# Performance work log

Measured on AMD Instinct MI355X. Metric: run time of the kernel, lower is better.

Reference implementation:

```python
import jax, jax.numpy as jnp
import numpy as np

B, T, C, H, N = 4, 1024, 2048, 32, 64
DFF, DW, DV, DA, DG = 8192, 64, 32, 64, 128
GN_EPS = 64e-5  # RWKV7 ln_x GroupNorm eps


def _ln(x, w, b, eps=1e-5):
    m = x.mean(-1, keepdims=True)
    v = ((x - m) ** 2).mean(-1, keepdims=True)
    return (x - m) / jnp.sqrt(v + eps) * w + b


def _block(x, v_first, att_shift, ffn_shift, wkv_state,
           ln1_w, ln1_b, ln2_w, ln2_b,
           x_r, x_w, x_k, x_v, x_a, x_g,
           Wr, Wk, Wv, Wo,
           w0, w1, w2, v0, v1, v2, a0, a1, a2, g1, g2,
           k_k, k_a, r_k, lnx_w, lnx_b,
           ffn_xk, Wk_ffn, Wv_ffn):
    # ----- TimeMix -----
    xn = _ln(x, ln1_w, ln1_b)
    xx = jnp.concatenate([att_shift[:, None, :], xn[:, :-1]], axis=1) - xn
    xr = xn + xx * x_r
    xw = xn + xx * x_w
    xk_ = xn + xx * x_k
    xv = xn + xx * x_v
    xa = xn + xx * x_a
    xg = xn + xx * x_g

    r = xr @ Wr
    w = -jax.nn.softplus(-(w0 + jnp.tanh(xw @ w1) @ w2)) - 0.5  # <= -0.5
    k = xk_ @ Wk
    v = xv @ Wv
    # layer_id != 0: interpolate toward v_first
    v = v + (v_first - v) * jax.nn.sigmoid(v0 + (xv @ v1) @ v2)
    a = jax.nn.sigmoid(a0 + (xa @ a1) @ a2)
    g = jax.nn.sigmoid(xg @ g1) @ g2

    kk = (k * k_k).reshape(B, T, H, N)
    kk = kk / jnp.maximum(jnp.linalg.norm(kk, axis=-1, keepdims=True), 1e-12)
    k = k * (1.0 + (a - 1.0) * k_a)

    rh = r.reshape(B, T, H, N)
    wh = jnp.exp(-jnp.exp(w.reshape(B, T, H, N)))  # decay in (0,1)
    kh = k.reshape(B, T, H, N)
    vh = v.reshape(B, T, H, N)
    ah = a.reshape(B, T, H, N)
    aa = -kk
    bb = kk * ah

    def step(S, inp):
        # S: [B,H,N(value),N(key)]
        r_t, w_t, k_t, v_t, a_t, b_t = inp
        sa = jnp.einsum('bhvk,bhk->bhv', S, a_t)
        S = S * w_t[:, :, None, :] + sa[..., None] * b_t[:, :, None, :] + v_t[..., None] * k_t[:, :, None, :]
        y = jnp.einsum('bhvk,bhk->bhv', S, r_t)
        return S, y

    tm = lambda z: jnp.swapaxes(z, 0, 1)  # [B,T,H,N] -> [T,B,H,N]
    S_new, ys = jax.lax.scan(step, wkv_state, (tm(rh), tm(wh), tm(kh), tm(vh), tm(aa), tm(bb)))
    x_wkv = jnp.swapaxes(ys, 0, 1).reshape(B, T, C)

    # GroupNorm over H groups of size N (RWKV7 ln_x)
    xh = x_wkv.reshape(B, T, H, N)
    mu = xh.mean(-1, keepdims=True)
    var = ((xh - mu) ** 2).mean(-1, keepdims=True)
    x_wkv = ((xh - mu) / jnp.sqrt(var + GN_EPS)).reshape(B, T, C) * lnx_w + lnx_b

    resid = ((rh * kh * r_k).sum(-1, keepdims=True) * vh).reshape(B, T, C)
    x_wkv = x_wkv + resid
    att_out = (x_wkv * g) @ Wo
    x1 = x + att_out

    # ----- ChannelMix -----
    xn2 = _ln(x1, ln2_w, ln2_b)
    xx2 = jnp.concatenate([ffn_shift[:, None, :], xn2[:, :-1]], axis=1) - xn2
    xkf = xn2 + xx2 * ffn_xk
    kf = jnp.square(jax.nn.relu(xkf @ Wk_ffn))
    x_out = x1 + kf @ Wv_ffn
    return x_out, S_new


def setup_inputs() -> dict:
    ks = jax.random.split(jax.random.key(0), 48)
    rn = lambda i, sh, s=1.0: jax.random.normal(ks[i], sh, dtype=jnp.float32) * s
    return {
        'x': rn(0, (B, T, C)), 'v_first': rn(1, (B, T, C)),
        'att_shift': rn(2, (B, C)), 'ffn_shift': rn(3, (B, C)),
        'wkv_state': jnp.zeros((B, H, N, N), jnp.float32),
        'ln1_w': jnp.ones((C,), jnp.float32), 'ln1_b': jnp.zeros((C,), jnp.float32),
        'ln2_w': jnp.ones((C,), jnp.float32), 'ln2_b': jnp.zeros((C,), jnp.float32),
        'x_r': rn(4, (C,), 0.3), 'x_w': rn(5, (C,), 0.3), 'x_k': rn(6, (C,), 0.3),
        'x_v': rn(7, (C,), 0.3), 'x_a': rn(8, (C,), 0.3), 'x_g': rn(9, (C,), 0.3),
        'Wr': rn(10, (C, C), 0.02), 'Wk': rn(11, (C, C), 0.02),
        'Wv': rn(12, (C, C), 0.02), 'Wo': rn(13, (C, C), 0.02),
        'w0': rn(14, (C,), 0.3), 'w1': rn(15, (C, DW), 0.02), 'w2': rn(16, (DW, C), 0.02),
        'v0': rn(17, (C,), 0.3), 'v1': rn(18, (C, DV), 0.02), 'v2': rn(19, (DV, C), 0.02),
        'a0': rn(20, (C,), 0.3), 'a1': rn(21, (C, DA), 0.02), 'a2': rn(22, (DA, C), 0.02),
        'g1': rn(23, (C, DG), 0.02), 'g2': rn(24, (DG, C), 0.02),
        'k_k': rn(25, (C,), 0.1) + 0.7, 'k_a': rn(26, (C,), 0.1) + 0.7, 'r_k': rn(27, (H, N), 0.1),
        'lnx_w': jnp.ones((C,), jnp.float32), 'lnx_b': jnp.zeros((C,), jnp.float32),
        'ffn_xk': rn(28, (C,), 0.3), 'Wk_ffn': rn(29, (C, DFF), 0.02), 'Wv_ffn': rn(30, (DFF, C), 0.02),
    }


def reference(x, v_first, att_shift, ffn_shift, wkv_state,
              ln1_w, ln1_b, ln2_w, ln2_b,
              x_r, x_w, x_k, x_v, x_a, x_g,
              Wr, Wk, Wv, Wo,
              w0, w1, w2, v0, v1, v2, a0, a1, a2, g1, g2,
              k_k, k_a, r_k, lnx_w, lnx_b,
              ffn_xk, Wk_ffn, Wv_ffn):
    return _block(x, v_first, att_shift, ffn_shift, wkv_state,
                  ln1_w, ln1_b, ln2_w, ln2_b,
                  x_r, x_w, x_k, x_v, x_a, x_g,
                  Wr, Wk, Wv, Wo,
                  w0, w1, w2, v0, v1, v2, a0, a1, a2, g1, g2,
                  k_k, k_a, r_k, lnx_w, lnx_b,
                  ffn_xk, Wk_ffn, Wv_ffn)
```

## Files before the change

kernel.cpp:

```cpp
#include <hip/hip_runtime.h>
#include <cstdint>


typedef __attribute__((ext_vector_type(4))) float f32x4;
typedef __attribute__((ext_vector_type(8))) __bf16 bf16x8;
typedef __attribute__((ext_vector_type(8))) unsigned short us8;

#define DEV __device__ __forceinline__

DEV unsigned short f2b(float f) {
  union { float f; unsigned u; } v; v.f = f;
  unsigned r = v.u + 0x7fffu + ((v.u >> 16) & 1u);
  return (unsigned short)(r >> 16);
}
DEV float b2f(unsigned short u) {
  union { unsigned u; float f; } v; v.u = (unsigned)u << 16;
  return v.f;
}

DEV void gload16(const void* g, void* l) {
  void* gg = const_cast<void*>(g);
  __builtin_amdgcn_global_load_lds(
      (__attribute__((address_space(1))) unsigned int*)gg,
      (__attribute__((address_space(3))) unsigned int*)l, 16, 0, 0);
}

DEV float red8(float v) {
  v += __shfl_xor(v, 1);
  v += __shfl_xor(v, 2);
  v += __shfl_xor(v, 4);
  return v;
}


__global__ void k_transpose(const float* __restrict__ src,
                            unsigned short* __restrict__ dst, int R, int Cc) {
  __shared__ float tile[32][33];
  const int c0 = blockIdx.x * 32, r0 = blockIdx.y * 32;
  const int tx = threadIdx.x, ty = threadIdx.y;
  for (int i = ty; i < 32; i += 8)
    tile[i][tx] = src[(size_t)(r0 + i) * Cc + c0 + tx];
  __syncthreads();
  for (int i = ty; i < 32; i += 8)
    dst[(size_t)(c0 + i) * R + r0 + tx] = f2b(tile[tx][i]);
}

__global__ void k_wcat(const float* __restrict__ w1, const float* __restrict__ a1,
                       const float* __restrict__ v1, const float* __restrict__ g1,
                       const float* __restrict__ xw, const float* __restrict__ xa,
                       const float* __restrict__ xv, const float* __restrict__ xg,
                       unsigned short* __restrict__ dst) {
  const int i = blockIdx.x * 256 + threadIdx.x;
  if (i >= 384 * 4096) return;
  const int j = i >> 12, c = i & 4095;
  float val = 0.f;
  if (j < 288) {
    const float* W; const float* mix; int jj, D;
    if (j < 64)       { W = w1; mix = xw; jj = j;       D = 64;  }
    else if (j < 128) { W = a1; mix = xa; jj = j - 64;  D = 64;  }
    else if (j < 160) { W = v1; mix = xv; jj = j - 128; D = 32;  }
    else              { W = g1; mix = xg; jj = j - 160; D = 128; }
    const int cc = c & 2047;
    val = W[(size_t)cc * D + jj];
    if (c >= 2048) val *= mix[cc];
  }
  dst[i] = f2b(val);
}


DEV void breduce2(float& a, float& b, float* rbuf) {
#pragma unroll
  for (int m = 1; m < 64; m <<= 1) { a += __shfl_xor(a, m); b += __shfl_xor(b, m); }
  const int wid = threadIdx.x >> 6, lane = threadIdx.x & 63;
  if (lane == 0) { rbuf[wid] = a; rbuf[4 + wid] = b; }
  __syncthreads();
  a = rbuf[0] + rbuf[1] + rbuf[2] + rbuf[3];
  b = rbuf[4] + rbuf[5] + rbuf[6] + rbuf[7];
  __syncthreads();
}

__global__ __launch_bounds__(256)
void k_ln1_mix(const float* __restrict__ x, const float* __restrict__ shift,
               const float* __restrict__ lw, const float* __restrict__ lb,
               const float* __restrict__ mr, const float* __restrict__ mk,
               const float* __restrict__ mv,
               unsigned short* __restrict__ A2, unsigned short* __restrict__ xrb,
               unsigned short* __restrict__ xkb, unsigned short* __restrict__ xvb) {
  __shared__ float rbuf[8];
  const int m = blockIdx.x, tid = threadIdx.x;
  const int b = m >> 10, t = m & 1023;
  const float* xt = x + (size_t)m * 2048 + tid * 8;
  const float* xp = (t > 0) ? (x + (size_t)(m - 1) * 2048 + tid * 8)
                            : (shift + (size_t)b * 2048 + tid * 8);
  float vt[8], vp[8];
  *(float4*)&vt[0] = *(const float4*)(xt);
  *(float4*)&vt[4] = *(const float4*)(xt + 4);
  *(float4*)&vp[0] = *(const float4*)(xp);
  *(float4*)&vp[4] = *(const float4*)(xp + 4);
  float st = 0.f, sp = 0.f;
#pragma unroll
  for (int i = 0; i < 8; ++i) { st += vt[i]; sp += vp[i]; }
  breduce2(st, sp, rbuf);
  const float mt_ = st * (1.f / 2048.f), mp_ = sp * (1.f / 2048.f);
  float qt = 0.f, qp = 0.f;
#pragma unroll
  for (int i = 0; i < 8; ++i) {
    float d0 = vt[i] - mt_; qt += d0 * d0;
    float d1 = vp[i] - mp_; qp += d1 * d1;
  }
  breduce2(qt, qp, rbuf);
  const float rt = rsqrtf(qt * (1.f / 2048.f) + 1e-5f);
  const float rp = rsqrtf(qp * (1.f / 2048.f) + 1e-5f);
  const bool lnp = (t > 0);
#pragma unroll
  for (int i = 0; i < 8; ++i) {
    const int c = tid * 8 + i;
    const float wv = lw[c], bv = lb[c];
    const float xn = (vt[i] - mt_) * rt * wv + bv;
    const float pn = lnp ? ((vp[i] - mp_) * rp * wv + bv) : vp[i];
    const float xx = pn - xn;
    A2[(size_t)m * 4096 + c] = f2b(xn);
    A2[(size_t)m * 4096 + 2048 + c] = f2b(xx);
    xrb[(size_t)m * 2048 + c] = f2b(xn + xx * mr[c]);
    xkb[(size_t)m * 2048 + c] = f2b(xn + xx * mk[c]);
    xvb[(size_t)m * 2048 + c] = f2b(xn + xx * mv[c]);
  }
}

__global__ __launch_bounds__(256)
void k_ln2_mix(const float* __restrict__ x1, const float* __restrict__ shift,
               const float* __restrict__ lw, const float* __restrict__ lb,
               const float* __restrict__ mk, unsigned short* __restrict__ xkf) {
  __shared__ float rbuf[8];
  const int m = blockIdx.x, tid = threadIdx.x;
  const int b = m >> 10, t = m & 1023;
  const float* xt = x1 + (size_t)m * 2048 + tid * 8;
  const float* xp = (t > 0) ? (x1 + (size_t)(m - 1) * 2048 + tid * 8)
                            : (shift + (size_t)b * 2048 + tid * 8);
  float vt[8], vp[8];
  *(float4*)&vt[0] = *(const float4*)(xt);
  *(float4*)&vt[4] = *(const float4*)(xt + 4);
  *(float4*)&vp[0] = *(const float4*)(xp);
  *(float4*)&vp[4] = *(const float4*)(xp + 4);
  float st = 0.f, sp = 0.f;
#pragma unroll
  for (int i = 0; i < 8; ++i) { st += vt[i]; sp += vp[i]; }
  breduce2(st, sp, rbuf);
  const float mt_ = st * (1.f / 2048.f), mp_ = sp * (1.f / 2048.f);
  float qt = 0.f, qp = 0.f;
#pragma unroll
  for (int i = 0; i < 8; ++i) {
    float d0 = vt[i] - mt_; qt += d0 * d0;
    float d1 = vp[i] - mp_; qp += d1 * d1;
  }
  breduce2(qt, qp, rbuf);
  const float rt = rsqrtf(qt * (1.f / 2048.f) + 1e-5f);
  const float rp = rsqrtf(qp * (1.f / 2048.f) + 1e-5f);
  const bool lnp = (t > 0);
#pragma unroll
  for (int i = 0; i < 8; ++i) {
    const int c = tid * 8 + i;
    const float wv = lw[c], bv = lb[c];
    const float xn = (vt[i] - mt_) * rt * wv + bv;
    const float pn = lnp ? ((vp[i] - mp_) * rp * wv + bv) : vp[i];
    xkf[(size_t)m * 2048 + c] = f2b(xn + (pn - xn) * mk[c]);
  }
}


constexpr int EP_F32 = 0, EP_B16 = 1, EP_W = 2, EP_AB16 = 3, EP_VGB16 = 4,
              EP_RELU2 = 5, EP_ADDF = 6, EP_HACT = 7;

template <int EP>
DEV void ep_store(float acc, long row, long c, long ldc, float* Co,
                  unsigned short* Cob, const float* bias, const float* e0f,
                  const unsigned short* e0b) {
  const long idx = row * ldc + c;
  if constexpr (EP == EP_F32) {
    Co[idx] = acc;
  } else if constexpr (EP == EP_B16) {
    Cob[idx] = f2b(acc);
  } else if constexpr (EP == EP_W) {
    const float wv = bias[c] + acc;
    const float sp = log1pf(expf(-wv));
    const float w = -sp - 0.5f;
    Co[idx] = expf(-expf(w));
  } else if constexpr (EP == EP_AB16) {
    Cob[idx] = f2b(1.f / (1.f + expf(-(bias[c] + acc))));
  } else if constexpr (EP == EP_VGB16) {
    const float s = 1.f / (1.f + expf(-(bias[c] + acc)));
    const float vv = b2f(e0b[idx]);
    Cob[idx] = f2b(vv + (e0f[idx] - vv) * s);
  } else if constexpr (EP == EP_RELU2) {
    const float r = fmaxf(acc, 0.f);
    Cob[idx] = f2b(r * r);
  } else if constexpr (EP == EP_ADDF) {
    Co[idx] = acc + e0f[idx];
  } else if constexpr (EP == EP_HACT) {
    float vv = acc;
    if (c < 64) vv = tanhf(vv);
    else if (c >= 160) vv = 1.f / (1.f + expf(-vv));
    Cob[idx] = f2b(vv);
  }
}

template <int EP>
__global__ __launch_bounds__(256)
void gemm_bt(const unsigned short* __restrict__ A, long lda,
             const unsigned short* __restrict__ Bt, long ldb, long N, long K,
             long ldc, float* __restrict__ Co, unsigned short* __restrict__ Cob,
             const float* __restrict__ bias, const float* __restrict__ e0f,
             const unsigned short* __restrict__ e0b) {
  __shared__ unsigned short As[4096];
  __shared__ unsigned short Bs[4096];
  const int tid = threadIdx.x;
  const int wid = tid >> 6, lane = tid & 63;
  const long row0 = (long)blockIdx.x * 128, col0 = (long)blockIdx.y * 128;
  const int wm = (wid >> 1) * 64, wn = (wid & 1) * 64;
  f32x4 acc[4][4] = {};
  const int sr = tid >> 2, sk = (tid & 3) * 8;
  const unsigned short* gA = A + (row0 + sr) * lda + sk;
  const unsigned short* gB = Bt + (col0 + sr) * ldb + sk;
  unsigned short* lA = As + wid * 512;
  unsigned short* lB = Bs + wid * 512;
  const int fr = lane & 15, fk = (lane >> 4) * 8;

  for (long kb = 0; kb < K; kb += 32) {
    gload16(gA + kb, lA);
    gload16(gA + kb + 64 * lda, lA + 2048);
    gload16(gB + kb, lB);
    gload16(gB + kb + 64 * ldb, lB + 2048);
    __syncthreads();
    bf16x8 af[4], bq[4];
#pragma unroll
    for (int mt = 0; mt < 4; ++mt)
      af[mt] = *(const bf16x8*)(As + (wm + mt * 16 + fr) * 32 + fk);
#pragma unroll
    for (int nt = 0; nt < 4; ++nt)
      bq[nt] = *(const bf16x8*)(Bs + (wn + nt * 16 + fr) * 32 + fk);
#pragma unroll
    for (int mt = 0; mt < 4; ++mt)
#pragma unroll
      for (int nt = 0; nt < 4; ++nt)
        acc[mt][nt] = __builtin_amdgcn_mfma_f32_16x16x32_bf16(
            af[mt], bq[nt], acc[mt][nt], 0, 0, 0);
    __syncthreads();
  }
  const int fq = lane >> 4;
#pragma unroll
  for (int mt = 0; mt < 4; ++mt) {
#pragma unroll
    for (int nt = 0; nt < 4; ++nt) {
      const long c = col0 + wn + nt * 16 + fr;
      if (c < N) {
        const long rb = row0 + wm + mt * 16 + fq * 4;
#pragma unroll
        for (int rg = 0; rg < 4; ++rg)
          ep_store<EP>(acc[mt][nt][rg], rb + rg, c, ldc, Co, Cob, bias, e0f, e0b);
      }
    }
  }
}

__global__ __launch_bounds__(256)
void k_post(unsigned short* __restrict__ kio, unsigned short* __restrict__ abio,
            unsigned short* __restrict__ aao, const float* __restrict__ kkw,
            const float* __restrict__ kaw) {
  const int m = blockIdx.x, tid = threadIdx.x;
  const size_t base = (size_t)m * 2048 + tid * 8;
  us8 k8 = *(const us8*)(kio + base);
  us8 a8 = *(const us8*)(abio + base);
  float kk8[8], ka8[8];
  *(float4*)&kk8[0] = *(const float4*)(kkw + tid * 8);
  *(float4*)&kk8[4] = *(const float4*)(kkw + tid * 8 + 4);
  *(float4*)&ka8[0] = *(const float4*)(kaw + tid * 8);
  *(float4*)&ka8[4] = *(const float4*)(kaw + tid * 8 + 4);
  float kx[8], kv[8], av[8];
  float ss = 0.f;
#pragma unroll
  for (int i = 0; i < 8; ++i) {
    kv[i] = b2f(k8[i]); av[i] = b2f(a8[i]);
    kx[i] = kv[i] * kk8[i]; ss += kx[i] * kx[i];
  }
  ss = red8(ss);
  const float inv = 1.f / fmaxf(sqrtf(ss), 1e-12f);
  us8 kh8, aa8, bb8;
#pragma unroll
  for (int i = 0; i < 8; ++i) {
    const float kkn = kx[i] * inv;
    kh8[i] = f2b(kv[i] * (1.f + (av[i] - 1.f) * ka8[i]));
    aa8[i] = f2b(-kkn);
    bb8[i] = f2b(kkn * av[i]);
  }
  *(us8*)(kio + base) = kh8;
  *(us8*)(aao + base) = aa8;
  *(us8*)(abio + base) = bb8;
}


DEV float red16(float x) {
  union { float f; int i; } a, r;
  a.f = x; r.i = __builtin_amdgcn_update_dpp(0, a.i, 0xB1, 0xf, 0xf, true);
  x += r.f;
  a.f = x; r.i = __builtin_amdgcn_update_dpp(0, a.i, 0x4E, 0xf, 0xf, true);
  x += r.f;
  a.f = x; r.i = __builtin_amdgcn_update_dpp(0, a.i, 0x124, 0xf, 0xf, true);
  x += r.f;
  a.f = x; r.i = __builtin_amdgcn_update_dpp(0, a.i, 0x128, 0xf, 0xf, true);
  x += r.f;
  return x;
}

DEV void cv4(const uint2 q, float* o) {
  union { unsigned u; float f; } t;
  t.u = q.x << 16;          o[0] = t.f;
  t.u = q.x & 0xffff0000u;  o[1] = t.f;
  t.u = q.y << 16;          o[2] = t.f;
  t.u = q.y & 0xffff0000u;  o[3] = t.f;
}

__global__ __launch_bounds__(64)
void k_scan(const unsigned short* __restrict__ rp,
            const unsigned short* __restrict__ kp,
            const unsigned short* __restrict__ vp,
            const float* __restrict__ wp,
            const unsigned short* __restrict__ ap,
            const unsigned short* __restrict__ bp,
            const float* __restrict__ s0, float* __restrict__ yout,
            float* __restrict__ snew) {
  __shared__ float ylds[1024][4];
  const int lane = threadIdx.x;
  const int bh = blockIdx.x & 127;
  const int rq = blockIdx.x >> 7;
  const int b = bh >> 5, h = bh & 31;
  const int kg = lane & 15, rl = lane >> 4;
  const int v = rq * 4 + rl, ks = kg * 4;
  const size_t off_bh = (size_t)b * 1024 * 2048 + (size_t)h * 64;

  const unsigned short* prb = rp + off_bh + ks;
  const unsigned short* pkb = kp + off_bh + ks;
  const unsigned short* pab = ap + off_bh + ks;
  const unsigned short* pbb = bp + off_bh + ks;
  const float*          pwb = wp + off_bh + ks;
  const unsigned short* pvb = vp + off_bh + v;

  float S[4];
  *(float4*)&S[0] = *(const float4*)(s0 + (((size_t)bh * 64 + v) * 64 + ks));

  uint2 r0_, k0_, a0_, b0_, r1_, k1_, a1_, b1_;
  uint2 r2_, k2_, a2_, b2_, r3_, k3_, a3_, b3_;
  uint2 r4_, k4_, a4_, b4_, r5_, k5_, a5_, b5_;
  uint2 r6_, k6_, a6_, b6_, r7_, k7_, a7_, b7_;
  float4 w0_, w1_, w2_, w3_, w4_, w5_, w6_, w7_;
  unsigned short f0_, f1_, f2_, f3_, f4_, f5_, f6_, f7_;

#define SLOAD(Br, Bk, Ba, Bb, Bw, Bf, T)                                     \
  {                                                                          \
    const size_t o_ = (size_t)(T) * 2048;                                    \
    Br = *(const uint2*)(prb + o_);  Bk = *(const uint2*)(pkb + o_);         \
    Ba = *(const uint2*)(pab + o_);  Bb = *(const uint2*)(pbb + o_);         \
    Bw = *(const float4*)(pwb + o_); Bf = pvb[o_];                           \
  }

  SLOAD(r0_, k0_, a0_, b0_, w0_, f0_, 0)
  SLOAD(r1_, k1_, a1_, b1_, w1_, f1_, 1)
  SLOAD(r2_, k2_, a2_, b2_, w2_, f2_, 2)
  SLOAD(r3_, k3_, a3_, b3_, w3_, f3_, 3)
  SLOAD(r4_, k4_, a4_, b4_, w4_, f4_, 4)
  SLOAD(r5_, k5_, a5_, b5_, w5_, f5_, 5)
  SLOAD(r6_, k6_, a6_, b6_, w6_, f6_, 6)
  SLOAD(r7_, k7_, a7_, b7_, w7_, f7_, 7)

#define SBODY(T, Br, Bk, Ba, Bb, Bw, Bf)                                     \
  {                                                                          \
    float rr[4], kk[4], av[4], bv[4];                                        \
    cv4(Br, rr); cv4(Bk, kk); cv4(Ba, av); cv4(Bb, bv);                      \
    const float4 wf = Bw;                                                    \
    const float vv = b2f(Bf);                                                \
    int tn_ = (T) + 8; if (tn_ > 1023) tn_ = 1023;                           \
    SLOAD(Br, Bk, Ba, Bb, Bw, Bf, tn_)                                       \
    float sa = S[0] * av[0] + S[1] * av[1] + S[2] * av[2] + S[3] * av[3];    \
    sa = red16(sa);                                                          \
    float y;                                                                 \
    S[0] = S[0] * wf.x + sa * bv[0] + vv * kk[0]; y  = S[0] * rr[0];         \
    S[1] = S[1] * wf.y + sa * bv[1] + vv * kk[1]; y += S[1] * rr[1];         \
    S[2] = S[2] * wf.z + sa * bv[2] + vv * kk[2]; y += S[2] * rr[2];         \
    S[3] = S[3] * wf.w + sa * bv[3] + vv * kk[3]; y += S[3] * rr[3];         \
    y = red16(y);                                                            \
    if (kg == 0) ylds[T][rl] = y;                                            \
  }

  for (int tb = 0; tb < 1024; tb += 8) {
    SBODY(tb + 0, r0_, k0_, a0_, b0_, w0_, f0_)
    SBODY(tb + 1, r1_, k1_, a1_, b1_, w1_, f1_)
    SBODY(tb + 2, r2_, k2_, a2_, b2_, w2_, f2_)
    SBODY(tb + 3, r3_, k3_, a3_, b3_, w3_, f3_)
    SBODY(tb + 4, r4_, k4_, a4_, b4_, w4_, f4_)
    SBODY(tb + 5, r5_, k5_, a5_, b5_, w5_, f5_)
    SBODY(tb + 6, r6_, k6_, a6_, b6_, w6_, f6_)
    SBODY(tb + 7, r7_, k7_, a7_, b7_, w7_, f7_)
  }
#undef SBODY
#undef SLOAD

  *(float4*)(snew + (((size_t)bh * 64 + v) * 64 + ks)) = *(const float4*)&S[0];
  __syncthreads();
#pragma unroll 4
  for (int it = 0; it < 16; ++it) {
    const int t = lane + it * 64;
    *(float4*)(yout + off_bh + (size_t)t * 2048 + rq * 4) =
        *(const float4*)&ylds[t][0];
  }
}


__global__ __launch_bounds__(256)
void k_gn(const float* __restrict__ y, const unsigned short* __restrict__ r,
          const unsigned short* __restrict__ kh, const unsigned short* __restrict__ vf,
          const unsigned short* __restrict__ g, const float* __restrict__ rk,
          const float* __restrict__ lw, const float* __restrict__ lb,
          unsigned short* __restrict__ ywg) {
  const int m = blockIdx.x, tid = threadIdx.x;
  const size_t base = (size_t)m * 2048 + tid * 8;
  float yv[8];
  *(float4*)&yv[0] = *(const float4*)(y + base);
  *(float4*)&yv[4] = *(const float4*)(y + base + 4);
  us8 r8 = *(const us8*)(r + base);
  us8 k8 = *(const us8*)(kh + base);
  us8 v8 = *(const us8*)(vf + base);
  us8 g8 = *(const us8*)(g + base);
  float rkv[8];
  *(float4*)&rkv[0] = *(const float4*)(rk + tid * 8);
  *(float4*)&rkv[4] = *(const float4*)(rk + tid * 8 + 4);
  float sy = 0.f, sd = 0.f;
#pragma unroll
  for (int i = 0; i < 8; ++i) {
    sy += yv[i];
    sd += b2f(r8[i]) * b2f(k8[i]) * rkv[i];
  }
  sy = red8(sy);
  sd = red8(sd);
  const float mu = sy * (1.f / 64.f);
  float sq = 0.f;
#pragma unroll
  for (int i = 0; i < 8; ++i) { const float d = yv[i] - mu; sq += d * d; }
  sq = red8(sq);
  const float rstd = rsqrtf(sq * (1.f / 64.f) + 64e-5f);
  us8 o8;
#pragma unroll
  for (int i = 0; i < 8; ++i) {
    const int c = tid * 8 + i;
    const float gn = (yv[i] - mu) * rstd * lw[c] + lb[c];
    o8[i] = f2b((gn + sd * b2f(v8[i])) * b2f(g8[i]));
  }
  *(us8*)(ywg + base) = o8;
}


extern "C" void kernel_launch(void* const* d_in, const int* in_sizes, int n_in,
                              void* d_out, int out_size, void* d_ws,
                              size_t ws_size, hipStream_t stream) {
  (void)in_sizes; (void)n_in; (void)out_size; (void)ws_size;
  const float* x         = (const float*)d_in[0];
  const float* v_first   = (const float*)d_in[1];
  const float* att_shift = (const float*)d_in[2];
  const float* ffn_shift = (const float*)d_in[3];
  const float* wkv0      = (const float*)d_in[4];
  const float* ln1w = (const float*)d_in[5];
  const float* ln1b = (const float*)d_in[6];
  const float* ln2w = (const float*)d_in[7];
  const float* ln2b = (const float*)d_in[8];
  const float* x_r = (const float*)d_in[9];
  const float* x_w = (const float*)d_in[10];
  const float* x_k = (const float*)d_in[11];
  const float* x_v = (const float*)d_in[12];
  const float* x_a = (const float*)d_in[13];
  const float* x_g = (const float*)d_in[14];
  const float* Wr = (const float*)d_in[15];
  const float* Wk = (const float*)d_in[16];
  const float* Wv = (const float*)d_in[17];
  const float* Wo = (const float*)d_in[18];
  const float* w0 = (const float*)d_in[19];
  const float* w1 = (const float*)d_in[20];
  const float* w2 = (const float*)d_in[21];
  const float* v0 = (const float*)d_in[22];
  const float* v1 = (const float*)d_in[23];
  const float* v2 = (const float*)d_in[24];
  const float* a0 = (const float*)d_in[25];
  const float* a1 = (const float*)d_in[26];
  const float* a2 = (const float*)d_in[27];
  const float* g1 = (const float*)d_in[28];
  const float* g2 = (const float*)d_in[29];
  const float* k_k = (const float*)d_in[30];
  const float* k_a = (const float*)d_in[31];
  const float* r_k = (const float*)d_in[32];
  const float* lnxw = (const float*)d_in[33];
  const float* lnxb = (const float*)d_in[34];
  const float* ffn_xk = (const float*)d_in[35];
  const float* Wkf = (const float*)d_in[36];
  const float* Wvf = (const float*)d_in[37];

  char* ws = (char*)d_ws;
  constexpr size_t OFF_TWR   = 0;
  constexpr size_t OFF_TWK   = 8388608;
  constexpr size_t OFF_TWV   = 16777216;
  constexpr size_t OFF_TWO   = 25165824;
  constexpr size_t OFF_TW2   = 33554432;
  constexpr size_t OFF_TA2   = 33816576;
  constexpr size_t OFF_TV2   = 34078720;
  constexpr size_t OFF_TG2   = 34209792;
  constexpr size_t OFF_TWCAT = 34734080;
  constexpr size_t OFF_HACT  = 37879808;
  constexpr size_t OFF_GBUF  = 40239104;
  constexpr size_t OFF_WH    = 57016320;
  constexpr size_t OFF_R     = 90570752;
  constexpr size_t OFF_KH    = 107347968;
  constexpr size_t OFF_VF    = 124125184;
  constexpr size_t OFF_AA    = 140902400;
  constexpr size_t OFF_BB    = 157679616;

  unsigned short* tWr = (unsigned short*)(ws + OFF_TWR);
  unsigned short* tWk = (unsigned short*)(ws + OFF_TWK);
  unsigned short* tWv = (unsigned short*)(ws + OFF_TWV);
  unsigned short* tWo = (unsigned short*)(ws + OFF_TWO);
  unsigned short* tw2 = (unsigned short*)(ws + OFF_TW2);
  unsigned short* ta2 = (unsigned short*)(ws + OFF_TA2);
  unsigned short* tv2 = (unsigned short*)(ws + OFF_TV2);
  unsigned short* tg2 = (unsigned short*)(ws + OFF_TG2);
  unsigned short* tWcat = (unsigned short*)(ws + OFF_TWCAT);
  unsigned short* Hact  = (unsigned short*)(ws + OFF_HACT);
  unsigned short* gbuf  = (unsigned short*)(ws + OFF_GBUF);
  unsigned short* tWvfh = (unsigned short*)(ws + OFF_GBUF);
  unsigned short* act2  = (unsigned short*)(ws + OFF_WH);
  float*          whb   = (float*)(ws + OFF_WH);
  unsigned short* ywg   = (unsigned short*)(ws + OFF_WH);
  unsigned short* kf    = (unsigned short*)(ws + OFF_WH);
  unsigned short* bxr   = (unsigned short*)(ws + OFF_AA);
  unsigned short* bxk   = (unsigned short*)(ws + OFF_BB);
  unsigned short* bxv   = (unsigned short*)(ws + OFF_VF);
  unsigned short* rbuf  = (unsigned short*)(ws + OFF_R);
  unsigned short* khb   = (unsigned short*)(ws + OFF_KH);
  unsigned short* vfb   = (unsigned short*)(ws + OFF_VF);
  unsigned short* aab   = (unsigned short*)(ws + OFF_AA);
  unsigned short* bbb   = (unsigned short*)(ws + OFF_BB);
  unsigned short* vraw  = (unsigned short*)(ws + OFF_AA);
  unsigned short* abuf  = (unsigned short*)(ws + OFF_BB);
  float*          x1    = (float*)(ws + OFF_R);
  unsigned short* xkf   = (unsigned short*)(ws + OFF_VF);
  unsigned short* tWkf  = (unsigned short*)(ws + OFF_AA);
  float* out = (float*)d_out;
  float* snew = out + 8388608;

  const dim3 tb(32, 8);
  k_transpose<<<dim3(64, 64), tb, 0, stream>>>(Wr, tWr, 2048, 2048);
  k_transpose<<<dim3(64, 64), tb, 0, stream>>>(Wk, tWk, 2048, 2048);
  k_transpose<<<dim3(64, 64), tb, 0, stream>>>(Wv, tWv, 2048, 2048);
  k_transpose<<<dim3(64, 64), tb, 0, stream>>>(Wo, tWo, 2048, 2048);
  k_transpose<<<dim3(64, 2), tb, 0, stream>>>(w2, tw2, 64, 2048);
  k_transpose<<<dim3(64, 2), tb, 0, stream>>>(a2, ta2, 64, 2048);
  k_transpose<<<dim3(64, 1), tb, 0, stream>>>(v2, tv2, 32, 2048);
  k_transpose<<<dim3(64, 4), tb, 0, stream>>>(g2, tg2, 128, 2048);
  k_wcat<<<6144, 256, 0, stream>>>(w1, a1, v1, g1, x_w, x_a, x_v, x_g, tWcat);

  k_ln1_mix<<<4096, 256, 0, stream>>>(x, att_shift, ln1w, ln1b, x_r, x_k, x_v,
                                      act2, bxr, bxk, bxv);
  gemm_bt<EP_B16><<<dim3(32, 16), 256, 0, stream>>>(
      bxr, 2048, tWr, 2048, 2048, 2048, 2048, nullptr, rbuf, nullptr, nullptr, nullptr);
  gemm_bt<EP_B16><<<dim3(32, 16), 256, 0, stream>>>(
      bxk, 2048, tWk, 2048, 2048, 2048, 2048, nullptr, khb, nullptr, nullptr, nullptr);
  gemm_bt<EP_B16><<<dim3(32, 16), 256, 0, stream>>>(
      bxv, 2048, tWv, 2048, 2048, 2048, 2048, nullptr, vraw, nullptr, nullptr, nullptr);
  gemm_bt<EP_HACT><<<dim3(32, 3), 256, 0, stream>>>(
      act2, 4096, tWcat, 4096, 288, 4096, 288, nullptr, Hact, nullptr, nullptr, nullptr);
  gemm_bt<EP_W><<<dim3(32, 16), 256, 0, stream>>>(
      Hact + 0, 288, tw2, 64, 2048, 64, 2048, whb, nullptr, w0, nullptr, nullptr);
  gemm_bt<EP_AB16><<<dim3(32, 16), 256, 0, stream>>>(
      Hact + 64, 288, ta2, 64, 2048, 64, 2048, nullptr, abuf, a0, nullptr, nullptr);
  gemm_bt<EP_VGB16><<<dim3(32, 16), 256, 0, stream>>>(
      Hact + 128, 288, tv2, 32, 2048, 32, 2048, nullptr, vfb, v0, v_first, vraw);
  gemm_bt<EP_B16><<<dim3(32, 16), 256, 0, stream>>>(
      Hact + 160, 288, tg2, 128, 2048, 128, 2048, nullptr, gbuf, nullptr, nullptr, nullptr);
  k_post<<<4096, 256, 0, stream>>>(khb, abuf, aab, k_k, k_a);

  k_scan<<<2048, 64, 0, stream>>>(rbuf, khb, vfb, whb, aab, bbb, wkv0, out, snew);
  k_gn<<<4096, 256, 0, stream>>>(out, rbuf, khb, vfb, gbuf, r_k, lnxw, lnxb, ywg);

  gemm_bt<EP_ADDF><<<dim3(32, 16), 256, 0, stream>>>(
      ywg, 2048, tWo, 2048, 2048, 2048, 2048, x1, nullptr, nullptr, x, nullptr);

  k_ln2_mix<<<4096, 256, 0, stream>>>(x1, ffn_shift, ln2w, ln2b, ffn_xk, xkf);
  k_transpose<<<dim3(256, 64), tb, 0, stream>>>(Wkf, tWkf, 2048, 8192);
  gemm_bt<EP_RELU2><<<dim3(32, 32), 256, 0, stream>>>(
      xkf, 2048, tWkf, 2048, 4096, 2048, 4096, nullptr, kf, nullptr, nullptr, nullptr);
  k_transpose<<<dim3(64, 128), tb, 0, stream>>>(Wvf, tWvfh, 4096, 2048);
  gemm_bt<EP_ADDF><<<dim3(32, 16), 256, 0, stream>>>(
      kf, 4096, tWvfh, 4096, 2048, 4096, 2048, out, nullptr, nullptr, x1, nullptr);
  gemm_bt<EP_RELU2><<<dim3(32, 32), 256, 0, stream>>>(
      xkf, 2048, tWkf + (size_t)4096 * 2048, 2048, 4096, 2048, 4096, nullptr, kf,
      nullptr, nullptr, nullptr);
  k_transpose<<<dim3(64, 128), tb, 0, stream>>>(Wvf + (size_t)4096 * 2048, tWvfh,
                                                4096, 2048);
  gemm_bt<EP_ADDF><<<dim3(32, 16), 256, 0, stream>>>(
      kf, 4096, tWvfh, 4096, 2048, 4096, 2048, out, nullptr, nullptr, out, nullptr);
}
```

Baseline: 1.416 ms.

## Stage scan inputs through LDS with async global_load_lds ring and bf16 output

The WKV scan kernel now prefetches each timestep's r/k/a/b/w/v rows into an 8-deep LDS ring with 49 lanes issuing 16-byte global_load_lds requests. This replaces the per-lane register prefetch of 8 timesteps and cuts the scattered small per-lane global loads and register pressure. The scan output y is also stored as bf16 instead of fp32, which halves the traffic into the GroupNorm kernel. The cost is an LDS round trip per step with manual waitcnt synchronization, which relies on wave-level ordering and drops the __syncthreads, plus reduced precision on y before normalization.

```diff
diff --git a/kernel.cpp b/kernel.cpp
--- a/kernel.cpp
+++ b/kernel.cpp
@@ -326,9 +326,10 @@
             const float* __restrict__ wp,
             const unsigned short* __restrict__ ap,
             const unsigned short* __restrict__ bp,
-            const float* __restrict__ s0, float* __restrict__ yout,
+            const float* __restrict__ s0, unsigned short* __restrict__ yout,
             float* __restrict__ snew) {
-  __shared__ float ylds[1024][4];
+  __shared__ float4 slots[8][49];
+  __shared__ unsigned short ylds[1024][4];
   const int lane = threadIdx.x;
   const int bh = blockIdx.x & 127;
   const int rq = blockIdx.x >> 7;
@@ -337,104 +338,93 @@
   const int v = rq * 4 + rl, ks = kg * 4;
   const size_t off_bh = (size_t)b * 1024 * 2048 + (size_t)h * 64;
 
-  const unsigned short* prb = rp + off_bh + ks;
-  const unsigned short* pkb = kp + off_bh + ks;
-  const unsigned short* pab = ap + off_bh + ks;
-  const unsigned short* pbb = bp + off_bh + ks;
-  const float*          pwb = wp + off_bh + ks;
-  const unsigned short* pvb = vp + off_bh + v;
-
   float S[4];
   *(float4*)&S[0] = *(const float4*)(s0 + (((size_t)bh * 64 + v) * 64 + ks));
 
-  uint2 r0_, k0_, a0_, b0_, r1_, k1_, a1_, b1_;
-  uint2 r2_, k2_, a2_, b2_, r3_, k3_, a3_, b3_;
-  uint2 r4_, k4_, a4_, b4_, r5_, k5_, a5_, b5_;
-  uint2 r6_, k6_, a6_, b6_, r7_, k7_, a7_, b7_;
-  float4 w0_, w1_, w2_, w3_, w4_, w5_, w6_, w7_;
-  unsigned short f0_, f1_, f2_, f3_, f4_, f5_, f6_, f7_;
-
-#define SLOAD(Br, Bk, Ba, Bb, Bw, Bf, T)                                     \
-  {                                                                          \
-    const size_t o_ = (size_t)(T) * 2048;                                    \
-    Br = *(const uint2*)(prb + o_);  Bk = *(const uint2*)(pkb + o_);         \
-    Ba = *(const uint2*)(pab + o_);  Bb = *(const uint2*)(pbb + o_);         \
-    Bw = *(const float4*)(pwb + o_); Bf = pvb[o_];                           \
-  }
-
-  SLOAD(r0_, k0_, a0_, b0_, w0_, f0_, 0)
-  SLOAD(r1_, k1_, a1_, b1_, w1_, f1_, 1)
-  SLOAD(r2_, k2_, a2_, b2_, w2_, f2_, 2)
-  SLOAD(r3_, k3_, a3_, b3_, w3_, f3_, 3)
-  SLOAD(r4_, k4_, a4_, b4_, w4_, f4_, 4)
-  SLOAD(r5_, k5_, a5_, b5_, w5_, f5_, 5)
-  SLOAD(r6_, k6_, a6_, b6_, w6_, f6_, 6)
-  SLOAD(r7_, k7_, a7_, b7_, w7_, f7_, 7)
-
-#define SBODY(T, Br, Bk, Ba, Bb, Bw, Bf)                                     \
-  {                                                                          \
-    float rr[4], kk[4], av[4], bv[4];                                        \
-    cv4(Br, rr); cv4(Bk, kk); cv4(Ba, av); cv4(Bb, bv);                      \
-    const float4 wf = Bw;                                                    \
-    const float vv = b2f(Bf);                                                \
-    int tn_ = (T) + 8; if (tn_ > 1023) tn_ = 1023;                           \
-    SLOAD(Br, Bk, Ba, Bb, Bw, Bf, tn_)                                       \
-    float sa = S[0] * av[0] + S[1] * av[1] + S[2] * av[2] + S[3] * av[3];    \
-    sa = red16(sa);                                                          \
-    float y;                                                                 \
-    S[0] = S[0] * wf.x + sa * bv[0] + vv * kk[0]; y  = S[0] * rr[0];         \
-    S[1] = S[1] * wf.y + sa * bv[1] + vv * kk[1]; y += S[1] * rr[1];         \
-    S[2] = S[2] * wf.z + sa * bv[2] + vv * kk[2]; y += S[2] * rr[2];         \
-    S[3] = S[3] * wf.w + sa * bv[3] + vv * kk[3]; y += S[3] * rr[3];         \
-    y = red16(y);                                                            \
-    if (kg == 0) ylds[T][rl] = y;                                            \
-  }
-
-  for (int tb = 0; tb < 1024; tb += 8) {
-    SBODY(tb + 0, r0_, k0_, a0_, b0_, w0_, f0_)
-    SBODY(tb + 1, r1_, k1_, a1_, b1_, w1_, f1_)
-    SBODY(tb + 2, r2_, k2_, a2_, b2_, w2_, f2_)
-    SBODY(tb + 3, r3_, k3_, a3_, b3_, w3_, f3_)
-    SBODY(tb + 4, r4_, k4_, a4_, b4_, w4_, f4_)
-    SBODY(tb + 5, r5_, k5_, a5_, b5_, w5_, f5_)
-    SBODY(tb + 6, r6_, k6_, a6_, b6_, w6_, f6_)
-    SBODY(tb + 7, r7_, k7_, a7_, b7_, w7_, f7_)
-  }
-#undef SBODY
-#undef SLOAD
+  const char* gp = nullptr;
+  size_t gstep = 0;
+  if (lane < 49) {
+    if (lane < 32) {
+      const int arr = lane >> 3, sub = lane & 7;
+      const unsigned short* base = arr == 0 ? rp : arr == 1 ? kp
+                                 : arr == 2 ? ap : bp;
+      gp = (const char*)(base + off_bh + sub * 8);
+      gstep = 4096;
+    } else if (lane < 48) {
+      gp = (const char*)(wp + off_bh + (lane - 32) * 4);
+      gstep = 8192;
+    } else {
+      gp = (const char*)(vp + off_bh + (rq & ~1) * 4);
+      gstep = 4096;
+    }
+  }
+#pragma unroll
+  for (int s = 0; s < 8; ++s) {
+    if (lane < 49) gload16(gp, &slots[s][0]);
+    gp += gstep;
+  }
+
+  for (int t = 0; t < 1024; ++t) {
+    asm volatile("s_waitcnt vmcnt(7)" ::: "memory");
+    const int sl = t & 7;
+    const char* sb = (const char*)&slots[sl][0];
+    uint2 r2 = *(const uint2*)(sb + kg * 8);
+    uint2 k2 = *(const uint2*)(sb + 128 + kg * 8);
+    uint2 a2 = *(const uint2*)(sb + 256 + kg * 8);
+    uint2 b2 = *(const uint2*)(sb + 384 + kg * 8);
+    float4 wf = *(const float4*)(sb + 512 + kg * 16);
+    const unsigned short vfu =
+        *(const unsigned short*)(sb + 768 + ((rq & 1) * 4 + rl) * 2);
+    asm volatile("s_waitcnt lgkmcnt(0)" ::: "memory");
+    if (lane < 49) gload16(gp, &slots[sl][0]);
+    if (t < 1015) gp += gstep;
+
+    float rr[4], kk[4], av[4], bv[4];
+    cv4(r2, rr); cv4(k2, kk); cv4(a2, av); cv4(b2, bv);
+    const float vv = b2f(vfu);
+    float sa = S[0] * av[0] + S[1] * av[1] + S[2] * av[2] + S[3] * av[3];
+    sa = red16(sa);
+    float y;
+    S[0] = S[0] * wf.x + sa * bv[0] + vv * kk[0]; y  = S[0] * rr[0];
+    S[1] = S[1] * wf.y + sa * bv[1] + vv * kk[1]; y += S[1] * rr[1];
+    S[2] = S[2] * wf.z + sa * bv[2] + vv * kk[2]; y += S[2] * rr[2];
+    S[3] = S[3] * wf.w + sa * bv[3] + vv * kk[3]; y += S[3] * rr[3];
+    y = red16(y);
+    if (kg == 0) ylds[t][rl] = f2b(y);
+  }
 
   *(float4*)(snew + (((size_t)bh * 64 + v) * 64 + ks)) = *(const float4*)&S[0];
-  __syncthreads();
+  asm volatile("s_waitcnt lgkmcnt(0)" ::: "memory");
 #pragma unroll 4
   for (int it = 0; it < 16; ++it) {
     const int t = lane + it * 64;
-    *(float4*)(yout + off_bh + (size_t)t * 2048 + rq * 4) =
-        *(const float4*)&ylds[t][0];
+    const uint2 val = *(const uint2*)&ylds[t][0];
+    *(uint2*)(yout + off_bh + (size_t)t * 2048 + rq * 4) = val;
   }
 }
 
 
 __global__ __launch_bounds__(256)
-void k_gn(const float* __restrict__ y, const unsigned short* __restrict__ r,
+void k_gn(const unsigned short* __restrict__ y, const unsigned short* __restrict__ r,
           const unsigned short* __restrict__ kh, const unsigned short* __restrict__ vf,
           const unsigned short* __restrict__ g, const float* __restrict__ rk,
           const float* __restrict__ lw, const float* __restrict__ lb,
           unsigned short* __restrict__ ywg) {
   const int m = blockIdx.x, tid = threadIdx.x;
   const size_t base = (size_t)m * 2048 + tid * 8;
-  float yv[8];
-  *(float4*)&yv[0] = *(const float4*)(y + base);
-  *(float4*)&yv[4] = *(const float4*)(y + base + 4);
+  us8 y8 = *(const us8*)(y + base);
   us8 r8 = *(const us8*)(r + base);
   us8 k8 = *(const us8*)(kh + base);
   us8 v8 = *(const us8*)(vf + base);
   us8 g8 = *(const us8*)(g + base);
+  float yv[8];
   float rkv[8];
   *(float4*)&rkv[0] = *(const float4*)(rk + tid * 8);
   *(float4*)&rkv[4] = *(const float4*)(rk + tid * 8 + 4);
   float sy = 0.f, sd = 0.f;
 #pragma unroll
   for (int i = 0; i < 8; ++i) {
+    yv[i] = b2f(y8[i]);
     sy += yv[i];
     sd += b2f(r8[i]) * b2f(k8[i]) * rkv[i];
   }
@@ -582,8 +572,10 @@
       Hact + 160, 288, tg2, 128, 2048, 128, 2048, nullptr, gbuf, nullptr, nullptr, nullptr);
   k_post<<<4096, 256, 0, stream>>>(khb, abuf, aab, k_k, k_a);
 
-  k_scan<<<2048, 64, 0, stream>>>(rbuf, khb, vfb, whb, aab, bbb, wkv0, out, snew);
-  k_gn<<<4096, 256, 0, stream>>>(out, rbuf, khb, vfb, gbuf, r_k, lnxw, lnxb, ywg);
+  k_scan<<<2048, 64, 0, stream>>>(rbuf, khb, vfb, whb, aab, bbb, wkv0,
+                                  (unsigned short*)out, snew);
+  k_gn<<<4096, 256, 0, stream>>>((const unsigned short*)out, rbuf, khb, vfb,
+                                 gbuf, r_k, lnxw, lnxb, ywg);
 
   gemm_bt<EP_ADDF><<<dim3(32, 16), 256, 0, stream>>>(
       ywg, 2048, tWo, 2048, 2048, 2048, 2048, x1, nullptr, nullptr, x, nullptr);
```

After: 1.355 ms. 4.3% less time.
